# Kernel tuning notes

Hardware: AMD Instinct MI355X
Metric: run time of the kernel (lower is better)

The kernel has to match this reference:

```python
import jax, jax.numpy as jnp
import numpy as np

EPS = 1e-5

def layer_norm(x, g, b):
    mu = jnp.mean(x, axis=-1, keepdims=True)
    var = jnp.mean(jnp.square(x - mu), axis=-1, keepdims=True)
    return (x - mu) * jax.lax.rsqrt(var + EPS) * g + b

def gather_recent(seq_tokens, seq_mask, count):
    # vectorized right-aligned gather of last `count` valid tokens per row
    B, S, D = seq_tokens.shape
    csum = jnp.cumsum(seq_mask.astype(jnp.int32), axis=1)          # [B,S]
    total = csum[:, -1:]                                           # [B,1]
    rank = total - csum                                            # 0 = last valid (at valid positions)
    sel = seq_mask & (rank < count)
    dest = jnp.where(sel, count - 1 - rank, count)                 # dump invalid into slot `count`
    b_idx = jnp.arange(B)[:, None]
    buf = jnp.zeros((B, count + 1, D), seq_tokens.dtype)
    recent = buf.at[b_idx, dest].set(seq_tokens * sel[..., None].astype(seq_tokens.dtype))[:, :count]
    recent_mask = jnp.arange(count)[None, :] >= (count - total)    # [B,count]
    return recent, recent_mask

def setup_inputs() -> dict:
    key = jax.random.key(0)
    B, S, D, H, P = 16, 2048, 1024, 16, 8
    ks = jax.random.split(key, 8)
    hidden_states = jax.random.normal(ks[0], (B, S, D), jnp.float32)
    lengths = jax.random.randint(ks[1], (B,), 1, S + 1)
    valid_mask = jnp.arange(S)[None, :] < lengths[:, None]
    s = 0.02
    return {
        "hidden_states": hidden_states,
        "valid_mask": valid_mask,
        "queries": jax.random.normal(ks[2], (P, D), jnp.float32) * s,
        "in_proj_w": jax.random.normal(ks[3], (3 * D, D), jnp.float32) * s,
        "in_proj_b": jnp.zeros((3 * D,), jnp.float32),
        "out_w": jax.random.normal(ks[4], (D, D), jnp.float32) * s,
        "out_b": jnp.zeros((D,), jnp.float32),
        "ln_pma_g": jnp.ones((D,), jnp.float32),
        "ln_pma_b": jnp.zeros((D,), jnp.float32),
        "ln_v_g": jnp.ones((D,), jnp.float32),
        "ln_v_b": jnp.zeros((D,), jnp.float32),
        "W_v": jax.random.normal(ks[5], (D, D), jnp.float32) * s,
        "b_v": jnp.zeros((D,), jnp.float32),
        "ln_g_g": jnp.ones((D,), jnp.float32),
        "ln_g_b": jnp.zeros((D,), jnp.float32),
        "W_g": jax.random.normal(ks[6], (D, D), jnp.float32) * s,
        "b_g": jnp.zeros((D,), jnp.float32),
        "cls_count": 1, "pma_count": 8, "recent_count": 64, "num_heads": 16,
    }

def reference(hidden_states, valid_mask, queries, in_proj_w, in_proj_b, out_w, out_b,
              ln_pma_g, ln_pma_b, ln_v_g, ln_v_b, W_v, b_v, ln_g_g, ln_g_b, W_g, b_g,
              cls_count, pma_count, recent_count, num_heads):
    B, S, D = hidden_states.shape
    H = num_heads
    hd = D // H
    # ---- PMA (torch nn.MultiheadAttention, batch_first, eval/no-dropout) ----
    Wq, Wk, Wv_ = in_proj_w[:D], in_proj_w[D:2 * D], in_proj_w[2 * D:]
    bq, bk, bv_ = in_proj_b[:D], in_proj_b[D:2 * D], in_proj_b[2 * D:]
    q = (queries @ Wq.T + bq)                       # [P, D]
    k = hidden_states @ Wk.T + bk                   # [B, S, D]
    v = hidden_states @ Wv_.T + bv_                 # [B, S, D]
    qh = q.reshape(pma_count, H, hd)                # [P, H, hd]
    kh = k.reshape(B, S, H, hd)
    vh = v.reshape(B, S, H, hd)
    scores = jnp.einsum('phd,bshd->bhps', qh, kh) / jnp.sqrt(jnp.asarray(hd, hidden_states.dtype))
    scores = jnp.where(valid_mask[:, None, None, :], scores, jnp.asarray(-1e9, scores.dtype))
    attn = jax.nn.softmax(scores, axis=-1)          # [B, H, P, S]
    ctx = jnp.einsum('bhps,bshd->bphd', attn, vh).reshape(B, pma_count, D)
    pooled = ctx @ out_w.T + out_b
    pma_tokens = layer_norm(queries[None, :, :] + pooled, ln_pma_g, ln_pma_b)  # [B, P, D]
    pma_mask = jnp.ones((B, pma_count), bool)
    # ---- split cls / sequence, gather recent ----
    cls_tokens = hidden_states[:, :cls_count]
    cls_mask = valid_mask[:, :cls_count]
    recent_tokens, recent_mask = gather_recent(hidden_states[:, cls_count:],
                                               valid_mask[:, cls_count:], recent_count)
    summary = jnp.concatenate([cls_tokens, pma_tokens, recent_tokens], axis=1)
    summary_mask = jnp.concatenate([cls_mask, pma_mask, recent_mask], axis=1)
    # ---- SiLU self-gating ----
    val = jax.nn.silu(layer_norm(summary, ln_v_g, ln_v_b) @ W_v.T + b_v)
    gate = jax.nn.sigmoid(layer_norm(summary, ln_g_g, ln_g_b) @ W_g.T + b_g)
    gated = gate * val * summary_mask[..., None].astype(summary.dtype)
    return gated, summary_mask
```

## Files before the change

kernel.cpp:

```cpp
#include <hip/hip_runtime.h>
#include <hip/hip_bf16.h>
#include <math.h>


#define Bn 16
#define Sn 2048
#define Dn 1024
#define Hn 16
#define Pn 8
#define Tn 73
#define RECn 64

typedef __attribute__((ext_vector_type(8))) short short8;
typedef __attribute__((ext_vector_type(4))) float f32x4;

__device__ __forceinline__ short f2bf(float x) {
    union { __hip_bfloat16 h; short s; } u;
    u.h = __float2bfloat16(x);
    return u.s;
}

__device__ __forceinline__ void gload_lds16(const void* g, void* l) {
    __builtin_amdgcn_global_load_lds((const __attribute__((address_space(1))) void*)g,
                                     (__attribute__((address_space(3))) void*)l, 16, 0, 0);
}

__device__ __forceinline__ int swzP(int row, int ks, int pitch) {
    return row * pitch + (ks ^ ((row & 7) << 3));
}

__global__ void detect_mask_kernel(const unsigned char* __restrict__ raw,
                                   int* __restrict__ flag) {
    __shared__ int any;
    if (threadIdx.x == 0) any = 0;
    __syncthreads();
    const uint4* r4 = (const uint4*)raw;
    int local = 0;
    for (int i = threadIdx.x; i < (Bn * Sn) / 16; i += blockDim.x) {
        uint4 w = r4[i];
        if ((w.x & 0xFFFFFF00u) | (w.y & 0xFFFFFF00u) |
            (w.z & 0xFFFFFF00u) | (w.w & 0xFFFFFF00u)) local = 1;
    }
    if (local) any = 1;
    __syncthreads();
    if (threadIdx.x == 0) *flag = any;
}

__global__ void canon_mask_kernel(const void* __restrict__ raw,
                                  const int* __restrict__ flag,
                                  unsigned char* __restrict__ canon) {
    int i = blockIdx.x * blockDim.x + threadIdx.x;
    if (i >= Bn * Sn) return;
    unsigned char v;
    if (*flag)
        v = ((const unsigned char*)raw)[i] ? 1 : 0;
    else
        v = ((const int*)raw)[i] ? 1 : 0;
    canon[i] = v;
}

__global__ void prep_kernel(const unsigned char* __restrict__ valid,
                            int* __restrict__ totals, int* __restrict__ rsrc,
                            float* __restrict__ maskf) {
    int b = blockIdx.x, t = threadIdx.x;
    const int SP = Sn - 1;
    __shared__ int lc[256];
    if (t < RECn) rsrc[b * RECn + t] = -1;

    int base = t * 8;
    unsigned char m[8];
    int cnt = 0;
#pragma unroll
    for (int i = 0; i < 8; i++) {
        int idx = base + i;
        m[i] = (idx < SP) ? valid[(size_t)b * Sn + 1 + idx] : (unsigned char)0;
        cnt += m[i] ? 1 : 0;
    }
    lc[t] = cnt;
    __syncthreads();
    for (int off = 1; off < 256; off <<= 1) {
        int add = (t >= off) ? lc[t - off] : 0;
        __syncthreads();
        lc[t] += add;
        __syncthreads();
    }
    int total = lc[255];
    int run = lc[t] - cnt;
#pragma unroll
    for (int i = 0; i < 8; i++) {
        if (m[i]) {
            run++;
            int rank = total - run;
            if (rank < RECn) rsrc[b * RECn + (RECn - 1 - rank)] = base + i + 1;
        }
    }
    if (t == 0) totals[b] = total;
    if (t < Tn) {
        float mv;
        if (t == 0) mv = valid[(size_t)b * Sn] ? 1.0f : 0.0f;
        else if (t < 1 + Pn) mv = 1.0f;
        else mv = ((t - 9) >= RECn - total) ? 1.0f : 0.0f;
        maskf[b * Tn + t] = mv;
    }
}

__global__ void q_kernel(const float* __restrict__ queries,
                         const float* __restrict__ in_w,
                         const float* __restrict__ in_b,
                         float* __restrict__ q) {
    int wid = (blockIdx.x * blockDim.x + threadIdx.x) >> 6;
    int lane = threadIdx.x & 63;
    if (wid >= Pn * Dn) return;
    int p = wid >> 10, j = wid & 1023;
    float acc = 0.0f;
    for (int c = lane; c < Dn; c += 64)
        acc += queries[p * Dn + c] * in_w[(size_t)j * Dn + c];
#pragma unroll
    for (int off = 32; off > 0; off >>= 1) acc += __shfl_down(acc, off);
    if (lane == 0) q[wid] = acc + in_b[j];
}

__global__ void A_kernel(const float* __restrict__ q,
                         const float* __restrict__ in_w,
                         const float* __restrict__ in_b,
                         short* __restrict__ Amat_bf, float* __restrict__ c0) {
    int h = blockIdx.x, cblk = blockIdx.y;
    int c = cblk * 256 + threadIdx.x;
    __shared__ float qs[8][64];
    for (int i = threadIdx.x; i < 512; i += 256) {
        int p = i >> 6, d = i & 63;
        qs[p][d] = q[p * Dn + h * 64 + d];
    }
    __syncthreads();
    float acc[8] = {};
#pragma unroll 8
    for (int d = 0; d < 64; d++) {
        float w = in_w[(size_t)(Dn + h * 64 + d) * Dn + c];
#pragma unroll
        for (int p = 0; p < 8; p++) acc[p] = fmaf(qs[p][d], w, acc[p]);
    }
#pragma unroll
    for (int p = 0; p < 8; p++)
        Amat_bf[(size_t)(h * 8 + p) * Dn + c] = f2bf(acc[p] * 0.125f);
    if (cblk == 0 && threadIdx.x < 8) {
        int p = threadIdx.x;
        float a = 0.0f;
        for (int d = 0; d < 64; d++) a += qs[p][d] * in_b[Dn + h * 64 + d];
        c0[h * 8 + p] = a * 0.125f;
    }
}

__global__ void wcvt_kernel(const float* __restrict__ w, short* __restrict__ wbf, int n) {
    int i = (blockIdx.x * blockDim.x + threadIdx.x) * 8;
    if (i >= n) return;
    f32x4 x0 = *(const f32x4*)(w + i);
    f32x4 x1 = *(const f32x4*)(w + i + 4);
    short8 o;
#pragma unroll
    for (int j = 0; j < 4; j++) { o[j] = f2bf(x0[j]); o[j + 4] = f2bf(x1[j]); }
    *(short8*)(wbf + i) = o;
}

__global__ __launch_bounds__(256) void scores_mfma(const float* __restrict__ hidden,
                                                   const short* __restrict__ Amat_bf,
                                                   const float* __restrict__ c0,
                                                   const unsigned char* __restrict__ valid,
                                                   float* __restrict__ scores) {
    __shared__ float Af[2][64 * 32];
    __shared__ short Bs[2][128 * 32];
    int tid = threadIdx.x, wave = tid >> 6, lane = tid & 63;
    int l15 = lane & 15, q = lane >> 4;
    int m0 = blockIdx.x * 64;
    int b = m0 >> 11, s_base = m0 & 2047;
    int ws = wave >> 1, wh = wave & 1;
    int s0 = ws * 32, hp0 = wh * 64;

    auto stage = [&](int bb, int k0) {
#pragma unroll
        for (int u = 0; u < 2; u++) {
            int i = tid + u * 256;
            int s = i >> 3, j = (i & 7) ^ (s & 7);
            gload_lds16(hidden + (size_t)(m0 + s) * Dn + k0 + j * 4, &Af[bb][i * 4]);
        }
#pragma unroll
        for (int u = 0; u < 2; u++) {
            int i = tid + u * 256;
            int hp = i >> 2, qq = (i & 3) ^ ((hp >> 1) & 3);
            gload_lds16(Amat_bf + (size_t)hp * Dn + k0 + qq * 8, &Bs[bb][i * 8]);
        }
    };

    f32x4 acc[2][4] = {};
    stage(0, 0);
    __syncthreads();

    for (int t = 0; t < 32; t++) {
        int bb = t & 1;
        if (t + 1 < 32) stage(bb ^ 1, (t + 1) * 32);
        short8 av[2], bv[4];
#pragma unroll
        for (int f = 0; f < 2; f++) {
            int s = s0 + f * 16 + l15;
            int base = s * 8;
            f32x4 lo = *(const f32x4*)&Af[bb][(base + ((2 * q) ^ (s & 7))) * 4];
            f32x4 hi = *(const f32x4*)&Af[bb][(base + ((2 * q + 1) ^ (s & 7))) * 4];
#pragma unroll
            for (int i = 0; i < 4; i++) { av[f][i] = f2bf(lo[i]); av[f][i + 4] = f2bf(hi[i]); }
        }
#pragma unroll
        for (int f = 0; f < 4; f++) {
            int hp = hp0 + f * 16 + l15;
            bv[f] = *(const short8*)&Bs[bb][(hp * 4 + (q ^ ((hp >> 1) & 3))) * 8];
        }
#pragma unroll
        for (int fa = 0; fa < 2; fa++)
#pragma unroll
            for (int fb = 0; fb < 4; fb++)
                acc[fa][fb] = __builtin_amdgcn_mfma_f32_16x16x32_bf16(av[fa], bv[fb], acc[fa][fb], 0, 0, 0);
        __syncthreads();
    }

#pragma unroll
    for (int fa = 0; fa < 2; fa++) {
        int srow = s_base + s0 + fa * 16 + q * 4;
        const unsigned char* vptr = valid + (size_t)b * Sn + srow;
        bool ok0 = vptr[0] != 0, ok1 = vptr[1] != 0, ok2 = vptr[2] != 0, ok3 = vptr[3] != 0;
#pragma unroll
        for (int fb = 0; fb < 4; fb++) {
            int hp = hp0 + fb * 16 + l15;
            float cc = c0[hp];
            f32x4 st;
            st[0] = ok0 ? acc[fa][fb][0] + cc : -1.0e9f;
            st[1] = ok1 ? acc[fa][fb][1] + cc : -1.0e9f;
            st[2] = ok2 ? acc[fa][fb][2] + cc : -1.0e9f;
            st[3] = ok3 ? acc[fa][fb][3] + cc : -1.0e9f;
            *(f32x4*)(scores + (size_t)(b * 128 + hp) * Sn + srow) = st;
        }
    }
}

__global__ __launch_bounds__(256) void softmax_kernel(const float* __restrict__ scores,
                                                      short* __restrict__ attn_bf) {
    const float* row = scores + (size_t)blockIdx.x * Sn;
    short* orow = attn_bf + (size_t)blockIdx.x * Sn;
    int t = threadIdx.x;
    __shared__ float red[256];
    f32x4 v0 = *(const f32x4*)(row + t * 8);
    f32x4 v1 = *(const f32x4*)(row + t * 8 + 4);
    float mx = -1.0e30f;
#pragma unroll
    for (int i = 0; i < 4; i++) { mx = fmaxf(mx, v0[i]); mx = fmaxf(mx, v1[i]); }
    red[t] = mx;
    __syncthreads();
    for (int off = 128; off > 0; off >>= 1) {
        if (t < off) red[t] = fmaxf(red[t], red[t + off]);
        __syncthreads();
    }
    mx = red[0];
    __syncthreads();
    float e[8];
    float sum = 0.0f;
#pragma unroll
    for (int i = 0; i < 4; i++) {
        e[i] = expf(v0[i] - mx); sum += e[i];
        e[i + 4] = expf(v1[i] - mx); sum += e[i + 4];
    }
    red[t] = sum;
    __syncthreads();
    for (int off = 128; off > 0; off >>= 1) {
        if (t < off) red[t] += red[t + off];
        __syncthreads();
    }
    float inv = 1.0f / red[0];
    short8 o;
#pragma unroll
    for (int i = 0; i < 8; i++) o[i] = f2bf(e[i] * inv);
    *(short8*)(orow + t * 8) = o;
}

__global__ __launch_bounds__(512) void U_mfma(const short* __restrict__ attn_bf,
                                              const float* __restrict__ hidden,
                                              float* __restrict__ Up0,
                                              float* __restrict__ Up1,
                                              float* __restrict__ Up2,
                                              float* __restrict__ Up3) {
    __shared__ short Hs[64 * 512];
    int n0 = blockIdx.x * 64, b = blockIdx.y, z = blockIdx.z;
    int zbase = z * 512;
    float* Up = (z == 0) ? Up0 : (z == 1) ? Up1 : (z == 2) ? Up2 : Up3;
    int tid = threadIdx.x, wave = tid >> 6, lane = tid & 63;
    int l15 = lane & 15, q = lane >> 4;

    {
        const float* src = hidden + ((size_t)b * Sn + zbase + tid) * Dn + n0;
#pragma unroll
        for (int c8 = 0; c8 < 64; c8 += 8) {
            f32x4 x = *(const f32x4*)(src + c8);
            f32x4 y = *(const f32x4*)(src + c8 + 4);
#pragma unroll
            for (int i = 0; i < 4; i++) {
                int c = c8 + i;
                Hs[c * 512 + (tid ^ ((c & 7) << 3))] = f2bf(x[i]);
            }
#pragma unroll
            for (int i = 0; i < 4; i++) {
                int c = c8 + 4 + i;
                Hs[c * 512 + (tid ^ ((c & 7) << 3))] = f2bf(y[i]);
            }
        }
    }
    __syncthreads();

    const short* ap = attn_bf + ((size_t)b * 128 + wave * 16 + l15) * Sn + zbase + q * 8;
    f32x4 acc[4] = {};
    short8 pa4[4];
#pragma unroll
    for (int d = 0; d < 4; d++) pa4[d] = *(const short8*)(ap + d * 32);
#pragma unroll
    for (int ic = 0; ic < 16; ic++) {
        short8 av = pa4[ic & 3];
        if (ic + 4 < 16) pa4[ic & 3] = *(const short8*)(ap + (ic + 4) * 32);
#pragma unroll
        for (int nf = 0; nf < 4; nf++) {
            short8 bv = *(const short8*)(&Hs[swzP(nf * 16 + l15, ic * 32 + q * 8, 512)]);
            acc[nf] = __builtin_amdgcn_mfma_f32_16x16x32_bf16(av, bv, acc[nf], 0, 0, 0);
        }
    }
    int hp = wave * 16 + q * 4;
#pragma unroll
    for (int nf = 0; nf < 4; nf++) {
        int c = n0 + nf * 16 + l15;
        float* up = Up + (size_t)(b * 128 + hp) * Dn + c;
#pragma unroll
        for (int r = 0; r < 4; r++) up[(size_t)r * Dn] = acc[nf][r];
    }
}

__global__ __launch_bounds__(64) void ctx_mfma(const float* __restrict__ Up0,
                                               const float* __restrict__ Up1,
                                               const float* __restrict__ Up2,
                                               const float* __restrict__ Up3,
                                               const float* __restrict__ in_w,
                                               const float* __restrict__ in_b,
                                               float* __restrict__ ctx) {
    int bh = blockIdx.x, b = bh >> 4, h = bh & 15;
    int lane = threadIdx.x & 63, l15 = lane & 15, koff = (lane >> 4) * 8;
    int p = l15 & 7;
    size_t uoff = ((size_t)b * 128 + h * 8 + p) * Dn + koff;
    const float* wv = in_w + (size_t)(2 * Dn + h * 64 + l15) * Dn + koff;
    f32x4 acc[4] = {};
    for (int k0 = 0; k0 < Dn; k0 += 32) {
        f32x4 a0 = *(const f32x4*)(Up0 + uoff + k0);
        f32x4 a1 = *(const f32x4*)(Up0 + uoff + k0 + 4);
        f32x4 b0 = *(const f32x4*)(Up1 + uoff + k0);
        f32x4 b1 = *(const f32x4*)(Up1 + uoff + k0 + 4);
        f32x4 d0 = *(const f32x4*)(Up2 + uoff + k0);
        f32x4 d1 = *(const f32x4*)(Up2 + uoff + k0 + 4);
        f32x4 e0 = *(const f32x4*)(Up3 + uoff + k0);
        f32x4 e1 = *(const f32x4*)(Up3 + uoff + k0 + 4);
        short8 av;
#pragma unroll
        for (int i = 0; i < 4; i++) {
            av[i] = f2bf((a0[i] + b0[i]) + (d0[i] + e0[i]));
            av[i + 4] = f2bf((a1[i] + b1[i]) + (d1[i] + e1[i]));
        }
#pragma unroll
        for (int nt = 0; nt < 4; nt++) {
            f32x4 w0 = *(const f32x4*)(wv + (size_t)nt * 16 * Dn + k0);
            f32x4 w1 = *(const f32x4*)(wv + (size_t)nt * 16 * Dn + k0 + 4);
            short8 bv;
#pragma unroll
            for (int i = 0; i < 4; i++) { bv[i] = f2bf(w0[i]); bv[i + 4] = f2bf(w1[i]); }
            acc[nt] = __builtin_amdgcn_mfma_f32_16x16x32_bf16(av, bv, acc[nt], 0, 0, 0);
        }
    }
    if (lane < 32) {
        int prow = (lane >> 4) * 4;
#pragma unroll
        for (int nt = 0; nt < 4; nt++) {
            int d = h * 64 + nt * 16 + l15;
            float bias = in_b[2 * Dn + d];
#pragma unroll
            for (int r = 0; r < 4; r++)
                ctx[(size_t)(b * 8 + prow + r) * Dn + d] = acc[nt][r] + bias;
        }
    }
}

__global__ __launch_bounds__(256) void pooled_mfma(const float* __restrict__ A,
                                                   const float* __restrict__ B,
                                                   const float* __restrict__ bias,
                                                   float* __restrict__ C, int M) {
    int wave = threadIdx.x >> 6, lane = threadIdx.x & 63;
    int l15 = lane & 15, koff = (lane >> 4) * 8;
    int m0 = blockIdx.x * 64 + (wave >> 1) * 32;
    int n0 = blockIdx.y * 64 + (wave & 1) * 32;
    f32x4 acc[2][2] = {};
    int ra0 = min(m0 + l15, M - 1);
    int ra1 = min(m0 + 16 + l15, M - 1);
    const float* a0p = A + (size_t)ra0 * Dn + koff;
    const float* a1p = A + (size_t)ra1 * Dn + koff;
    const float* b0p = B + (size_t)(n0 + l15) * Dn + koff;
    const float* b1p = B + (size_t)(n0 + 16 + l15) * Dn + koff;
    for (int k0 = 0; k0 < Dn; k0 += 32) {
        short8 av0, av1, bv0, bv1;
        f32x4 x, y;
        x = *(const f32x4*)(a0p + k0); y = *(const f32x4*)(a0p + k0 + 4);
#pragma unroll
        for (int i = 0; i < 4; i++) { av0[i] = f2bf(x[i]); av0[i + 4] = f2bf(y[i]); }
        x = *(const f32x4*)(a1p + k0); y = *(const f32x4*)(a1p + k0 + 4);
#pragma unroll
        for (int i = 0; i < 4; i++) { av1[i] = f2bf(x[i]); av1[i + 4] = f2bf(y[i]); }
        x = *(const f32x4*)(b0p + k0); y = *(const f32x4*)(b0p + k0 + 4);
#pragma unroll
        for (int i = 0; i < 4; i++) { bv0[i] = f2bf(x[i]); bv0[i + 4] = f2bf(y[i]); }
        x = *(const f32x4*)(b1p + k0); y = *(const f32x4*)(b1p + k0 + 4);
#pragma unroll
        for (int i = 0; i < 4; i++) { bv1[i] = f2bf(x[i]); bv1[i + 4] = f2bf(y[i]); }
        acc[0][0] = __builtin_amdgcn_mfma_f32_16x16x32_bf16(av0, bv0, acc[0][0], 0, 0, 0);
        acc[0][1] = __builtin_amdgcn_mfma_f32_16x16x32_bf16(av0, bv1, acc[0][1], 0, 0, 0);
        acc[1][0] = __builtin_amdgcn_mfma_f32_16x16x32_bf16(av1, bv0, acc[1][0], 0, 0, 0);
        acc[1][1] = __builtin_amdgcn_mfma_f32_16x16x32_bf16(av1, bv1, acc[1][1], 0, 0, 0);
    }
#pragma unroll
    for (int mf = 0; mf < 2; mf++) {
        int row0 = m0 + mf * 16 + (lane >> 4) * 4;
#pragma unroll
        for (int nf = 0; nf < 2; nf++) {
            int col = n0 + nf * 16 + l15;
            float bval = bias[col];
#pragma unroll
            for (int r = 0; r < 4; r++) {
                int row = row0 + r;
                if (row < M) C[(size_t)row * Dn + col] = acc[mf][nf][r] + bval;
            }
        }
    }
}

__global__ __launch_bounds__(256) void wgemm_mfma(const short* __restrict__ Abf,
                                                  const short* __restrict__ Bbf,
                                                  const float* __restrict__ bias,
                                                  float* __restrict__ C, int M) {
    int wave = threadIdx.x >> 6, lane = threadIdx.x & 63;
    int m0 = blockIdx.x * 64 + (wave >> 1) * 32;
    int n0 = blockIdx.y * 64 + (wave & 1) * 32;
    int koff = (lane >> 4) * 8;
    f32x4 acc[2][2] = {};
    int ra0 = min(m0 + (lane & 15), M - 1);
    int ra1 = min(m0 + 16 + (lane & 15), M - 1);
    const short* a0p = Abf + (size_t)ra0 * Dn + koff;
    const short* a1p = Abf + (size_t)ra1 * Dn + koff;
    const short* b0p = Bbf + (size_t)(n0 + (lane & 15)) * Dn + koff;
    const short* b1p = Bbf + (size_t)(n0 + 16 + (lane & 15)) * Dn + koff;
    for (int k0 = 0; k0 < Dn; k0 += 32) {
        short8 av0 = *(const short8*)(a0p + k0);
        short8 av1 = *(const short8*)(a1p + k0);
        short8 bv0 = *(const short8*)(b0p + k0);
        short8 bv1 = *(const short8*)(b1p + k0);
        acc[0][0] = __builtin_amdgcn_mfma_f32_16x16x32_bf16(av0, bv0, acc[0][0], 0, 0, 0);
        acc[0][1] = __builtin_amdgcn_mfma_f32_16x16x32_bf16(av0, bv1, acc[0][1], 0, 0, 0);
        acc[1][0] = __builtin_amdgcn_mfma_f32_16x16x32_bf16(av1, bv0, acc[1][0], 0, 0, 0);
        acc[1][1] = __builtin_amdgcn_mfma_f32_16x16x32_bf16(av1, bv1, acc[1][1], 0, 0, 0);
    }
#pragma unroll
    for (int mf = 0; mf < 2; mf++) {
        int row0 = m0 + mf * 16 + (lane >> 4) * 4;
#pragma unroll
        for (int nf = 0; nf < 2; nf++) {
            int col = n0 + nf * 16 + (lane & 15);
            float bval = bias[col];
#pragma unroll
            for (int r = 0; r < 4; r++) {
                int row = row0 + r;
                if (row < M) C[(size_t)row * Dn + col] = acc[mf][nf][r] + bval;
            }
        }
    }
}

__device__ __forceinline__ float block_sum(float v, float* red) {
    int tid = threadIdx.x;
    red[tid] = v;
    __syncthreads();
    for (int off = 128; off > 0; off >>= 1) {
        if (tid < off) red[tid] += red[tid + off];
        __syncthreads();
    }
    float r = red[0];
    __syncthreads();
    return r;
}

__global__ void summary_ln_kernel(const float* __restrict__ hidden,
                                  const float* __restrict__ queries,
                                  const float* __restrict__ pooled,
                                  const int* __restrict__ rsrc,
                                  const float* __restrict__ gpma, const float* __restrict__ bpma,
                                  const float* __restrict__ gv, const float* __restrict__ bv,
                                  const float* __restrict__ gg, const float* __restrict__ bg,
                                  short* __restrict__ lnv, short* __restrict__ lng) {
    __shared__ float red[256];
    int b = blockIdx.x, t = blockIdx.y, tid = threadIdx.x;
    float x[4];
    if (t == 0) {
#pragma unroll
        for (int i = 0; i < 4; i++)
            x[i] = hidden[(size_t)b * Sn * Dn + tid + i * 256];
    } else if (t < 1 + Pn) {
        int p = t - 1;
#pragma unroll
        for (int i = 0; i < 4; i++) {
            int c = tid + i * 256;
            x[i] = queries[p * Dn + c] + pooled[((size_t)b * Pn + p) * Dn + c];
        }
    } else {
        int src = rsrc[b * RECn + (t - 9)];
        if (src >= 0) {
#pragma unroll
            for (int i = 0; i < 4; i++)
                x[i] = hidden[((size_t)b * Sn + src) * Dn + tid + i * 256];
        } else {
#pragma unroll
            for (int i = 0; i < 4; i++) x[i] = 0.0f;
        }
    }
    if (t >= 1 && t < 1 + Pn) {
        float mu = block_sum(x[0] + x[1] + x[2] + x[3], red) * (1.0f / Dn);
        float d2 = 0.0f;
#pragma unroll
        for (int i = 0; i < 4; i++) { float d = x[i] - mu; d2 += d * d; }
        float inv = rsqrtf(block_sum(d2, red) * (1.0f / Dn) + 1e-5f);
#pragma unroll
        for (int i = 0; i < 4; i++) {
            int c = tid + i * 256;
            x[i] = (x[i] - mu) * inv * gpma[c] + bpma[c];
        }
    }
    float mu = block_sum(x[0] + x[1] + x[2] + x[3], red) * (1.0f / Dn);
    float d2 = 0.0f;
#pragma unroll
    for (int i = 0; i < 4; i++) { float d = x[i] - mu; d2 += d * d; }
    float inv = rsqrtf(block_sum(d2, red) * (1.0f / Dn) + 1e-5f);
    size_t row = (size_t)(b * Tn + t) * Dn;
#pragma unroll
    for (int i = 0; i < 4; i++) {
        int c = tid + i * 256;
        float xh = (x[i] - mu) * inv;
        lnv[row + c] = f2bf(xh * gv[c] + bv[c]);
        lng[row + c] = f2bf(xh * gg[c] + bg[c]);
    }
}

__global__ void gated_kernel(const float* __restrict__ c1, const float* __restrict__ c2,
                             const float* __restrict__ maskf, float* __restrict__ out) {
    int gi = blockIdx.x * blockDim.x + threadIdx.x;
    int row = gi >> 10;
    float m = maskf[row];
    float a = c1[gi], g = c2[gi];
    float sv = a / (1.0f + expf(-a));
    float sg = 1.0f / (1.0f + expf(-g));
    out[gi] = sg * sv * m;
}

extern "C" void kernel_launch(void* const* d_in, const int* in_sizes, int n_in,
                              void* d_out, int out_size, void* d_ws, size_t ws_size,
                              hipStream_t stream) {
    const float* hidden = (const float*)d_in[0];
    const void* valid_raw = d_in[1];
    const float* queries = (const float*)d_in[2];
    const float* in_w = (const float*)d_in[3];
    const float* in_b = (const float*)d_in[4];
    const float* out_w = (const float*)d_in[5];
    const float* out_b = (const float*)d_in[6];
    const float* ln_pma_g = (const float*)d_in[7];
    const float* ln_pma_b = (const float*)d_in[8];
    const float* ln_v_g = (const float*)d_in[9];
    const float* ln_v_b = (const float*)d_in[10];
    const float* W_v = (const float*)d_in[11];
    const float* b_v = (const float*)d_in[12];
    const float* ln_g_g = (const float*)d_in[13];
    const float* ln_g_b = (const float*)d_in[14];
    const float* W_g = (const float*)d_in[15];
    const float* b_g = (const float*)d_in[16];

    float* ws = (float*)d_ws;
    float* out = (float*)d_out;

    float* SC      = ws;
    short* attn_bf = (short*)(ws + 4194304);
    float* Up0     = ws;
    float* Up1     = ws + 2097152;
    float* Up2     = ws + 6291456;
    float* Up3     = ws + 8388608;
    float* qbuf    = ws + 10485760;
    short* Amat_bf = (short*)(ws + 10493952);
    float* c0      = ws + 10559488;
    float* ctx     = ws + 10559744;
    float* pooled  = ws + 10690816;
    short* Wv_bf   = (short*)(ws + 10821888);
    short* Wg_bf   = (short*)(ws + 11346176);
    int*   ivals   = (int*)(ws + 11870464);
    int* totals = ivals;
    int* rsrc = ivals + 16;
    int* flag = ivals + 16 + 1024;
    unsigned char* canon = (unsigned char*)(ivals + 16 + 1024 + 16);
    short* lnv_bf = (short*)ws;
    short* lng_bf = (short*)(ws + 622592);
    float* c1 = ws + 1245184;
    float* c2 = ws + 2441216;
    float* maskf = out + (size_t)Bn * Tn * Dn;

    const int M2 = Bn * Tn;

    detect_mask_kernel<<<1, 256, 0, stream>>>((const unsigned char*)valid_raw, flag);
    canon_mask_kernel<<<(Bn * Sn) / 256, 256, 0, stream>>>(valid_raw, flag, canon);
    prep_kernel<<<Bn, 256, 0, stream>>>(canon, totals, rsrc, maskf);
    q_kernel<<<(Pn * Dn) / 4, 256, 0, stream>>>(queries, in_w, in_b, qbuf);
    A_kernel<<<dim3(Hn, 4), 256, 0, stream>>>(qbuf, in_w, in_b, Amat_bf, c0);
    wcvt_kernel<<<512, 256, 0, stream>>>(W_v, Wv_bf, Dn * Dn);
    wcvt_kernel<<<512, 256, 0, stream>>>(W_g, Wg_bf, Dn * Dn);
    scores_mfma<<<(Bn * Sn) / 64, 256, 0, stream>>>(hidden, Amat_bf, c0, canon, SC);
    softmax_kernel<<<Bn * 128, 256, 0, stream>>>(SC, attn_bf);
    U_mfma<<<dim3(16, Bn, 4), 512, 0, stream>>>(attn_bf, hidden, Up0, Up1, Up2, Up3);
    ctx_mfma<<<Bn * Hn, 64, 0, stream>>>(Up0, Up1, Up2, Up3, in_w, in_b, ctx);
    pooled_mfma<<<dim3(2, 16), 256, 0, stream>>>(ctx, out_w, out_b, pooled, Bn * Pn);
    summary_ln_kernel<<<dim3(Bn, Tn), 256, 0, stream>>>(hidden, queries, pooled, rsrc,
                                                        ln_pma_g, ln_pma_b, ln_v_g, ln_v_b,
                                                        ln_g_g, ln_g_b, lnv_bf, lng_bf);
    wgemm_mfma<<<dim3((M2 + 63) / 64, 16), 256, 0, stream>>>(lnv_bf, Wv_bf, b_v, c1, M2);
    wgemm_mfma<<<dim3((M2 + 63) / 64, 16), 256, 0, stream>>>(lng_bf, Wg_bf, b_g, c2, M2);
    gated_kernel<<<(Bn * Tn * Dn) / 256, 256, 0, stream>>>(c1, c2, maskf, out);
}
```

Measured before the change: 249.3 us.

## Merge setup kernels, drop mask canonicalization, store U partials as bf16, fuse gate GEMMs

```diff
diff --git a/kernel.cpp b/kernel.cpp
--- a/kernel.cpp
+++ b/kernel.cpp
@@ -19,6 +19,14 @@
     u.h = __float2bfloat16(x);
     return u.s;
 }
+__device__ __forceinline__ float bf2f(short s) {
+    return __uint_as_float(((unsigned)(unsigned short)s) << 16);
+}
+
+__device__ __forceinline__ bool mask_at(const void* raw, int f, size_t idx) {
+    return f ? (((const unsigned char*)raw)[idx] != 0)
+             : (((const int*)raw)[idx] != 0);
+}
 
 __device__ __forceinline__ void gload_lds16(const void* g, void* l) {
     __builtin_amdgcn_global_load_lds((const __attribute__((address_space(1))) void*)g,
@@ -29,85 +37,28 @@
     return row * pitch + (ks ^ ((row & 7) << 3));
 }
 
-__global__ void detect_mask_kernel(const unsigned char* __restrict__ raw,
-                                   int* __restrict__ flag) {
-    __shared__ int any;
-    if (threadIdx.x == 0) any = 0;
-    __syncthreads();
-    const uint4* r4 = (const uint4*)raw;
-    int local = 0;
-    for (int i = threadIdx.x; i < (Bn * Sn) / 16; i += blockDim.x) {
-        uint4 w = r4[i];
-        if ((w.x & 0xFFFFFF00u) | (w.y & 0xFFFFFF00u) |
-            (w.z & 0xFFFFFF00u) | (w.w & 0xFFFFFF00u)) local = 1;
-    }
-    if (local) any = 1;
-    __syncthreads();
-    if (threadIdx.x == 0) *flag = any;
-}
-
-__global__ void canon_mask_kernel(const void* __restrict__ raw,
-                                  const int* __restrict__ flag,
-                                  unsigned char* __restrict__ canon) {
-    int i = blockIdx.x * blockDim.x + threadIdx.x;
-    if (i >= Bn * Sn) return;
-    unsigned char v;
-    if (*flag)
-        v = ((const unsigned char*)raw)[i] ? 1 : 0;
-    else
-        v = ((const int*)raw)[i] ? 1 : 0;
-    canon[i] = v;
-}
-
-__global__ void prep_kernel(const unsigned char* __restrict__ valid,
-                            int* __restrict__ totals, int* __restrict__ rsrc,
-                            float* __restrict__ maskf) {
-    int b = blockIdx.x, t = threadIdx.x;
-    const int SP = Sn - 1;
-    __shared__ int lc[256];
-    if (t < RECn) rsrc[b * RECn + t] = -1;
-
-    int base = t * 8;
-    unsigned char m[8];
-    int cnt = 0;
-#pragma unroll
-    for (int i = 0; i < 8; i++) {
-        int idx = base + i;
-        m[i] = (idx < SP) ? valid[(size_t)b * Sn + 1 + idx] : (unsigned char)0;
-        cnt += m[i] ? 1 : 0;
-    }
-    lc[t] = cnt;
-    __syncthreads();
-    for (int off = 1; off < 256; off <<= 1) {
-        int add = (t >= off) ? lc[t - off] : 0;
-        __syncthreads();
-        lc[t] += add;
-        __syncthreads();
-    }
-    int total = lc[255];
-    int run = lc[t] - cnt;
-#pragma unroll
-    for (int i = 0; i < 8; i++) {
-        if (m[i]) {
-            run++;
-            int rank = total - run;
-            if (rank < RECn) rsrc[b * RECn + (RECn - 1 - rank)] = base + i + 1;
-        }
-    }
-    if (t == 0) totals[b] = total;
-    if (t < Tn) {
-        float mv;
-        if (t == 0) mv = valid[(size_t)b * Sn] ? 1.0f : 0.0f;
-        else if (t < 1 + Pn) mv = 1.0f;
-        else mv = ((t - 9) >= RECn - total) ? 1.0f : 0.0f;
-        maskf[b * Tn + t] = mv;
-    }
-}
-
-__global__ void q_kernel(const float* __restrict__ queries,
-                         const float* __restrict__ in_w,
-                         const float* __restrict__ in_b,
-                         float* __restrict__ q) {
+__global__ __launch_bounds__(256) void setup1_kernel(const float* __restrict__ queries,
+                                                     const float* __restrict__ in_w,
+                                                     const float* __restrict__ in_b,
+                                                     const unsigned char* __restrict__ raw,
+                                                     float* __restrict__ q,
+                                                     int* __restrict__ flag) {
+    if (blockIdx.x == 2048) {
+        __shared__ int any;
+        if (threadIdx.x == 0) any = 0;
+        __syncthreads();
+        const uint4* r4 = (const uint4*)raw;
+        int local = 0;
+        for (int i = threadIdx.x; i < (Bn * Sn) / 16; i += blockDim.x) {
+            uint4 w = r4[i];
+            if ((w.x & 0xFFFFFF00u) | (w.y & 0xFFFFFF00u) |
+                (w.z & 0xFFFFFF00u) | (w.w & 0xFFFFFF00u)) local = 1;
+        }
+        if (local) any = 1;
+        __syncthreads();
+        if (threadIdx.x == 0) *flag = any;
+        return;
+    }
     int wid = (blockIdx.x * blockDim.x + threadIdx.x) >> 6;
     int lane = threadIdx.x & 63;
     if (wid >= Pn * Dn) return;
@@ -120,51 +71,90 @@
     if (lane == 0) q[wid] = acc + in_b[j];
 }
 
-__global__ void A_kernel(const float* __restrict__ q,
-                         const float* __restrict__ in_w,
-                         const float* __restrict__ in_b,
-                         short* __restrict__ Amat_bf, float* __restrict__ c0) {
-    int h = blockIdx.x, cblk = blockIdx.y;
-    int c = cblk * 256 + threadIdx.x;
+__global__ __launch_bounds__(256) void setup2_kernel(const float* __restrict__ q,
+                                                     const float* __restrict__ in_w,
+                                                     const float* __restrict__ in_b,
+                                                     const void* __restrict__ raw,
+                                                     const int* __restrict__ flag,
+                                                     short* __restrict__ Amat_bf,
+                                                     float* __restrict__ c0,
+                                                     int* __restrict__ totals,
+                                                     int* __restrict__ rsrc,
+                                                     float* __restrict__ maskf) {
     __shared__ float qs[8][64];
-    for (int i = threadIdx.x; i < 512; i += 256) {
-        int p = i >> 6, d = i & 63;
-        qs[p][d] = q[p * Dn + h * 64 + d];
-    }
-    __syncthreads();
-    float acc[8] = {};
+    __shared__ int lc[256];
+    if (blockIdx.x < 64) {
+        int h = blockIdx.x >> 2, cblk = blockIdx.x & 3;
+        int c = cblk * 256 + threadIdx.x;
+        for (int i = threadIdx.x; i < 512; i += 256) {
+            int p = i >> 6, d = i & 63;
+            qs[p][d] = q[p * Dn + h * 64 + d];
+        }
+        __syncthreads();
+        float acc[8] = {};
 #pragma unroll 8
-    for (int d = 0; d < 64; d++) {
-        float w = in_w[(size_t)(Dn + h * 64 + d) * Dn + c];
-#pragma unroll
-        for (int p = 0; p < 8; p++) acc[p] = fmaf(qs[p][d], w, acc[p]);
-    }
-#pragma unroll
-    for (int p = 0; p < 8; p++)
-        Amat_bf[(size_t)(h * 8 + p) * Dn + c] = f2bf(acc[p] * 0.125f);
-    if (cblk == 0 && threadIdx.x < 8) {
-        int p = threadIdx.x;
-        float a = 0.0f;
-        for (int d = 0; d < 64; d++) a += qs[p][d] * in_b[Dn + h * 64 + d];
-        c0[h * 8 + p] = a * 0.125f;
-    }
-}
-
-__global__ void wcvt_kernel(const float* __restrict__ w, short* __restrict__ wbf, int n) {
-    int i = (blockIdx.x * blockDim.x + threadIdx.x) * 8;
-    if (i >= n) return;
-    f32x4 x0 = *(const f32x4*)(w + i);
-    f32x4 x1 = *(const f32x4*)(w + i + 4);
-    short8 o;
-#pragma unroll
-    for (int j = 0; j < 4; j++) { o[j] = f2bf(x0[j]); o[j + 4] = f2bf(x1[j]); }
-    *(short8*)(wbf + i) = o;
+        for (int d = 0; d < 64; d++) {
+            float w = in_w[(size_t)(Dn + h * 64 + d) * Dn + c];
+#pragma unroll
+            for (int p = 0; p < 8; p++) acc[p] = fmaf(qs[p][d], w, acc[p]);
+        }
+#pragma unroll
+        for (int p = 0; p < 8; p++)
+            Amat_bf[(size_t)(h * 8 + p) * Dn + c] = f2bf(acc[p] * 0.125f);
+        if (cblk == 0 && threadIdx.x < 8) {
+            int p = threadIdx.x;
+            float a = 0.0f;
+            for (int d = 0; d < 64; d++) a += qs[p][d] * in_b[Dn + h * 64 + d];
+            c0[h * 8 + p] = a * 0.125f;
+        }
+        return;
+    }
+    int b = blockIdx.x - 64, t = threadIdx.x;
+    int f = *flag;
+    const int SP = Sn - 1;
+    if (t < RECn) rsrc[b * RECn + t] = -1;
+    int base = t * 8;
+    unsigned char m[8];
+    int cnt = 0;
+#pragma unroll
+    for (int i = 0; i < 8; i++) {
+        int idx = base + i;
+        m[i] = (idx < SP) ? (mask_at(raw, f, (size_t)b * Sn + 1 + idx) ? 1 : 0) : 0;
+        cnt += m[i];
+    }
+    lc[t] = cnt;
+    __syncthreads();
+    for (int off = 1; off < 256; off <<= 1) {
+        int add = (t >= off) ? lc[t - off] : 0;
+        __syncthreads();
+        lc[t] += add;
+        __syncthreads();
+    }
+    int total = lc[255];
+    int run = lc[t] - cnt;
+#pragma unroll
+    for (int i = 0; i < 8; i++) {
+        if (m[i]) {
+            run++;
+            int rank = total - run;
+            if (rank < RECn) rsrc[b * RECn + (RECn - 1 - rank)] = base + i + 1;
+        }
+    }
+    if (t == 0) totals[b] = total;
+    if (t < Tn) {
+        float mv;
+        if (t == 0) mv = mask_at(raw, f, (size_t)b * Sn) ? 1.0f : 0.0f;
+        else if (t < 1 + Pn) mv = 1.0f;
+        else mv = ((t - 9) >= RECn - total) ? 1.0f : 0.0f;
+        maskf[b * Tn + t] = mv;
+    }
 }
 
 __global__ __launch_bounds__(256) void scores_mfma(const float* __restrict__ hidden,
                                                    const short* __restrict__ Amat_bf,
                                                    const float* __restrict__ c0,
-                                                   const unsigned char* __restrict__ valid,
+                                                   const void* __restrict__ raw,
+                                                   const int* __restrict__ flag,
                                                    float* __restrict__ scores) {
     __shared__ float Af[2][64 * 32];
     __shared__ short Bs[2][128 * 32];
@@ -220,11 +210,13 @@
         __syncthreads();
     }
 
+    int fl = *flag;
 #pragma unroll
     for (int fa = 0; fa < 2; fa++) {
         int srow = s_base + s0 + fa * 16 + q * 4;
-        const unsigned char* vptr = valid + (size_t)b * Sn + srow;
-        bool ok0 = vptr[0] != 0, ok1 = vptr[1] != 0, ok2 = vptr[2] != 0, ok3 = vptr[3] != 0;
+        size_t vbase = (size_t)b * Sn + srow;
+        bool ok0 = mask_at(raw, fl, vbase), ok1 = mask_at(raw, fl, vbase + 1);
+        bool ok2 = mask_at(raw, fl, vbase + 2), ok3 = mask_at(raw, fl, vbase + 3);
 #pragma unroll
         for (int fb = 0; fb < 4; fb++) {
             int hp = hp0 + fb * 16 + l15;
@@ -280,14 +272,14 @@
 
 __global__ __launch_bounds__(512) void U_mfma(const short* __restrict__ attn_bf,
                                               const float* __restrict__ hidden,
-                                              float* __restrict__ Up0,
-                                              float* __restrict__ Up1,
-                                              float* __restrict__ Up2,
-                                              float* __restrict__ Up3) {
+                                              short* __restrict__ Up0,
+                                              short* __restrict__ Up1,
+                                              short* __restrict__ Up2,
+                                              short* __restrict__ Up3) {
     __shared__ short Hs[64 * 512];
     int n0 = blockIdx.x * 64, b = blockIdx.y, z = blockIdx.z;
     int zbase = z * 512;
-    float* Up = (z == 0) ? Up0 : (z == 1) ? Up1 : (z == 2) ? Up2 : Up3;
+    short* Up = (z == 0) ? Up0 : (z == 1) ? Up1 : (z == 2) ? Up2 : Up3;
     int tid = threadIdx.x, wave = tid >> 6, lane = tid & 63;
     int l15 = lane & 15, q = lane >> 4;
 
@@ -330,16 +322,16 @@
 #pragma unroll
     for (int nf = 0; nf < 4; nf++) {
         int c = n0 + nf * 16 + l15;
-        float* up = Up + (size_t)(b * 128 + hp) * Dn + c;
-#pragma unroll
-        for (int r = 0; r < 4; r++) up[(size_t)r * Dn] = acc[nf][r];
-    }
-}
-
-__global__ __launch_bounds__(64) void ctx_mfma(const float* __restrict__ Up0,
-                                               const float* __restrict__ Up1,
-                                               const float* __restrict__ Up2,
-                                               const float* __restrict__ Up3,
+        short* up = Up + (size_t)(b * 128 + hp) * Dn + c;
+#pragma unroll
+        for (int r = 0; r < 4; r++) up[(size_t)r * Dn] = f2bf(acc[nf][r]);
+    }
+}
+
+__global__ __launch_bounds__(64) void ctx_mfma(const short* __restrict__ Up0,
+                                               const short* __restrict__ Up1,
+                                               const short* __restrict__ Up2,
+                                               const short* __restrict__ Up3,
                                                const float* __restrict__ in_w,
                                                const float* __restrict__ in_b,
                                                float* __restrict__ ctx) {
@@ -350,20 +342,14 @@
     const float* wv = in_w + (size_t)(2 * Dn + h * 64 + l15) * Dn + koff;
     f32x4 acc[4] = {};
     for (int k0 = 0; k0 < Dn; k0 += 32) {
-        f32x4 a0 = *(const f32x4*)(Up0 + uoff + k0);
-        f32x4 a1 = *(const f32x4*)(Up0 + uoff + k0 + 4);
-        f32x4 b0 = *(const f32x4*)(Up1 + uoff + k0);
-        f32x4 b1 = *(const f32x4*)(Up1 + uoff + k0 + 4);
-        f32x4 d0 = *(const f32x4*)(Up2 + uoff + k0);
-        f32x4 d1 = *(const f32x4*)(Up2 + uoff + k0 + 4);
-        f32x4 e0 = *(const f32x4*)(Up3 + uoff + k0);
-        f32x4 e1 = *(const f32x4*)(Up3 + uoff + k0 + 4);
+        short8 s0 = *(const short8*)(Up0 + uoff + k0);
+        short8 s1 = *(const short8*)(Up1 + uoff + k0);
+        short8 s2 = *(const short8*)(Up2 + uoff + k0);
+        short8 s3 = *(const short8*)(Up3 + uoff + k0);
         short8 av;
 #pragma unroll
-        for (int i = 0; i < 4; i++) {
-            av[i] = f2bf((a0[i] + b0[i]) + (d0[i] + e0[i]));
-            av[i + 4] = f2bf((a1[i] + b1[i]) + (d1[i] + e1[i]));
-        }
+        for (int i = 0; i < 8; i++)
+            av[i] = f2bf((bf2f(s0[i]) + bf2f(s1[i])) + (bf2f(s2[i]) + bf2f(s3[i])));
 #pragma unroll
         for (int nt = 0; nt < 4; nt++) {
             f32x4 w0 = *(const f32x4*)(wv + (size_t)nt * 16 * Dn + k0);
@@ -438,26 +424,41 @@
     }
 }
 
-__global__ __launch_bounds__(256) void wgemm_mfma(const short* __restrict__ Abf,
-                                                  const short* __restrict__ Bbf,
-                                                  const float* __restrict__ bias,
-                                                  float* __restrict__ C, int M) {
+__global__ __launch_bounds__(256) void wgemm_mfma(const short* __restrict__ lnv,
+                                                  const short* __restrict__ lng,
+                                                  const float* __restrict__ Wv,
+                                                  const float* __restrict__ Wg,
+                                                  const float* __restrict__ bv_,
+                                                  const float* __restrict__ bg_,
+                                                  float* __restrict__ c1,
+                                                  float* __restrict__ c2, int M) {
+    int z = blockIdx.z;
+    const short* Abf = z ? lng : lnv;
+    const float* Bw = z ? Wg : Wv;
+    const float* bias = z ? bg_ : bv_;
+    float* C = z ? c2 : c1;
     int wave = threadIdx.x >> 6, lane = threadIdx.x & 63;
+    int l15 = lane & 15, koff = (lane >> 4) * 8;
     int m0 = blockIdx.x * 64 + (wave >> 1) * 32;
     int n0 = blockIdx.y * 64 + (wave & 1) * 32;
-    int koff = (lane >> 4) * 8;
     f32x4 acc[2][2] = {};
-    int ra0 = min(m0 + (lane & 15), M - 1);
-    int ra1 = min(m0 + 16 + (lane & 15), M - 1);
+    int ra0 = min(m0 + l15, M - 1);
+    int ra1 = min(m0 + 16 + l15, M - 1);
     const short* a0p = Abf + (size_t)ra0 * Dn + koff;
     const short* a1p = Abf + (size_t)ra1 * Dn + koff;
-    const short* b0p = Bbf + (size_t)(n0 + (lane & 15)) * Dn + koff;
-    const short* b1p = Bbf + (size_t)(n0 + 16 + (lane & 15)) * Dn + koff;
+    const float* b0p = Bw + (size_t)(n0 + l15) * Dn + koff;
+    const float* b1p = Bw + (size_t)(n0 + 16 + l15) * Dn + koff;
     for (int k0 = 0; k0 < Dn; k0 += 32) {
         short8 av0 = *(const short8*)(a0p + k0);
         short8 av1 = *(const short8*)(a1p + k0);
-        short8 bv0 = *(const short8*)(b0p + k0);
-        short8 bv1 = *(const short8*)(b1p + k0);
+        short8 bv0, bv1;
+        f32x4 x, y;
+        x = *(const f32x4*)(b0p + k0); y = *(const f32x4*)(b0p + k0 + 4);
+#pragma unroll
+        for (int i = 0; i < 4; i++) { bv0[i] = f2bf(x[i]); bv0[i + 4] = f2bf(y[i]); }
+        x = *(const f32x4*)(b1p + k0); y = *(const f32x4*)(b1p + k0 + 4);
+#pragma unroll
+        for (int i = 0; i < 4; i++) { bv1[i] = f2bf(x[i]); bv1[i + 4] = f2bf(y[i]); }
         acc[0][0] = __builtin_amdgcn_mfma_f32_16x16x32_bf16(av0, bv0, acc[0][0], 0, 0, 0);
         acc[0][1] = __builtin_amdgcn_mfma_f32_16x16x32_bf16(av0, bv1, acc[0][1], 0, 0, 0);
         acc[1][0] = __builtin_amdgcn_mfma_f32_16x16x32_bf16(av1, bv0, acc[1][0], 0, 0, 0);
@@ -468,7 +469,7 @@
         int row0 = m0 + mf * 16 + (lane >> 4) * 4;
 #pragma unroll
         for (int nf = 0; nf < 2; nf++) {
-            int col = n0 + nf * 16 + (lane & 15);
+            int col = n0 + nf * 16 + l15;
             float bval = bias[col];
 #pragma unroll
             for (int r = 0; r < 4; r++) {
@@ -589,22 +590,19 @@
 
     float* SC      = ws;
     short* attn_bf = (short*)(ws + 4194304);
-    float* Up0     = ws;
-    float* Up1     = ws + 2097152;
-    float* Up2     = ws + 6291456;
-    float* Up3     = ws + 8388608;
+    short* Up0     = (short*)ws;
+    short* Up1     = (short*)(ws + 1048576);
+    short* Up2     = (short*)(ws + 2097152);
+    short* Up3     = (short*)(ws + 3145728);
     float* qbuf    = ws + 10485760;
     short* Amat_bf = (short*)(ws + 10493952);
     float* c0      = ws + 10559488;
     float* ctx     = ws + 10559744;
     float* pooled  = ws + 10690816;
-    short* Wv_bf   = (short*)(ws + 10821888);
-    short* Wg_bf   = (short*)(ws + 11346176);
     int*   ivals   = (int*)(ws + 11870464);
     int* totals = ivals;
     int* rsrc = ivals + 16;
     int* flag = ivals + 16 + 1024;
-    unsigned char* canon = (unsigned char*)(ivals + 16 + 1024 + 16);
     short* lnv_bf = (short*)ws;
     short* lng_bf = (short*)(ws + 622592);
     float* c1 = ws + 1245184;
@@ -613,14 +611,11 @@
 
     const int M2 = Bn * Tn;
 
-    detect_mask_kernel<<<1, 256, 0, stream>>>((const unsigned char*)valid_raw, flag);
-    canon_mask_kernel<<<(Bn * Sn) / 256, 256, 0, stream>>>(valid_raw, flag, canon);
-    prep_kernel<<<Bn, 256, 0, stream>>>(canon, totals, rsrc, maskf);
-    q_kernel<<<(Pn * Dn) / 4, 256, 0, stream>>>(queries, in_w, in_b, qbuf);
-    A_kernel<<<dim3(Hn, 4), 256, 0, stream>>>(qbuf, in_w, in_b, Amat_bf, c0);
-    wcvt_kernel<<<512, 256, 0, stream>>>(W_v, Wv_bf, Dn * Dn);
-    wcvt_kernel<<<512, 256, 0, stream>>>(W_g, Wg_bf, Dn * Dn);
-    scores_mfma<<<(Bn * Sn) / 64, 256, 0, stream>>>(hidden, Amat_bf, c0, canon, SC);
+    setup1_kernel<<<2049, 256, 0, stream>>>(queries, in_w, in_b,
+                                            (const unsigned char*)valid_raw, qbuf, flag);
+    setup2_kernel<<<80, 256, 0, stream>>>(qbuf, in_w, in_b, valid_raw, flag,
+                                          Amat_bf, c0, totals, rsrc, maskf);
+    scores_mfma<<<(Bn * Sn) / 64, 256, 0, stream>>>(hidden, Amat_bf, c0, valid_raw, flag, SC);
     softmax_kernel<<<Bn * 128, 256, 0, stream>>>(SC, attn_bf);
     U_mfma<<<dim3(16, Bn, 4), 512, 0, stream>>>(attn_bf, hidden, Up0, Up1, Up2, Up3);
     ctx_mfma<<<Bn * Hn, 64, 0, stream>>>(Up0, Up1, Up2, Up3, in_w, in_b, ctx);
@@ -628,7 +623,7 @@
     summary_ln_kernel<<<dim3(Bn, Tn), 256, 0, stream>>>(hidden, queries, pooled, rsrc,
                                                         ln_pma_g, ln_pma_b, ln_v_g, ln_v_b,
                                                         ln_g_g, ln_g_b, lnv_bf, lng_bf);
-    wgemm_mfma<<<dim3((M2 + 63) / 64, 16), 256, 0, stream>>>(lnv_bf, Wv_bf, b_v, c1, M2);
-    wgemm_mfma<<<dim3((M2 + 63) / 64, 16), 256, 0, stream>>>(lng_bf, Wg_bf, b_g, c2, M2);
+    wgemm_mfma<<<dim3((M2 + 63) / 64, 16, 2), 256, 0, stream>>>(lnv_bf, lng_bf, W_v, W_g,
+                                                                b_v, b_g, c1, c2, M2);
     gated_kernel<<<(Bn * Tn * Dn) / 256, 256, 0, stream>>>(c1, c2, maskf, out);
 }
```

After: 234.6 us. -5.9%, faster.
